# Kernel tuning notes

Measured on AMD Instinct MI355X. Metric: run time of the kernel, lower is better.

Reference implementation:

```python
import jax, jax.numpy as jnp
import numpy as np

N, U, V = 512, 2048, 43          # batch, phoneme seq len, vocab (Phoneme43)
H, K, NCLASS = 512, 10, 512      # hidden, GMM components, 2**bit
EPS = 1e-5


def gru_cell(x, h, wih, whh, bih, bhh):
    # PyTorch GRU gate order: r, z, n
    gi = x @ wih.T + bih          # [N, 3H]
    gh = h @ whh.T + bhh          # [N, 3H]
    gi_r, gi_z, gi_n = jnp.split(gi, 3, axis=1)
    gh_r, gh_z, gh_n = jnp.split(gh, 3, axis=1)
    r = jax.nn.sigmoid(gi_r + gh_r)
    z = jax.nn.sigmoid(gi_z + gh_z)
    n = jnp.tanh(gi_n + r * gh_n)
    return (1.0 - z) * n + z * h


def setup_inputs() -> dict:
    key = jax.random.key(0)
    ks = jax.random.split(key, 20)
    s = 0.05  # keep exp() arguments tame
    inp = {
        "xt": jax.random.normal(ks[0], (N,), jnp.float32),
        "cx": jax.random.uniform(ks[1], (N, U, V), jnp.float32),
        "encoder_hidden": jax.random.normal(ks[2], (1, N, H), jnp.float32),
        "wt_1": jax.random.normal(ks[3], (N, V), jnp.float32) * s,
        "h2t_1": jax.random.normal(ks[4], (1, N, H), jnp.float32),
        "h3t_1": jax.random.uniform(ks[5], (1, N, H), jnp.float32),
        "kappa_t_1": jax.random.uniform(ks[6], (N, K), jnp.float32),
        # learned params
        "Wh1p_w": jax.random.normal(ks[7], (3 * K, H + V), jnp.float32) * s,
        "Wh1p_b": jax.random.normal(ks[8], (3 * K,), jnp.float32) * s,
        "rnn2_wih": jax.random.normal(ks[9], (3 * H, 1 + V), jnp.float32) * s,
        "rnn2_whh": jax.random.normal(ks[10], (3 * H, H), jnp.float32) * s,
        "rnn2_bih": jax.random.normal(ks[11], (3 * H,), jnp.float32) * s,
        "rnn2_bhh": jax.random.normal(ks[12], (3 * H,), jnp.float32) * s,
        "rnn3_wih": jax.random.normal(ks[13], (3 * H, H), jnp.float32) * s,
        "rnn3_whh": jax.random.normal(ks[14], (3 * H, H), jnp.float32) * s,
        "rnn3_bih": jax.random.normal(ks[15], (3 * H,), jnp.float32) * s,
        "rnn3_bhh": jax.random.normal(ks[16], (3 * H,), jnp.float32) * s,
        "Y_w": jax.random.normal(ks[17], (NCLASS, H), jnp.float32) * s,
        "Y_b": jax.random.normal(ks[18], (NCLASS,), jnp.float32) * s,
    }
    return inp


def reference(xt, cx, encoder_hidden, wt_1, h2t_1, h3t_1, kappa_t_1,
              Wh1p_w, Wh1p_b, rnn2_wih, rnn2_whh, rnn2_bih, rnn2_bhh,
              rnn3_wih, rnn3_whh, rnn3_bih, rnn3_bhh, Y_w, Y_b):
    eh = encoder_hidden[0]                                   # [N, H]
    abk = jnp.concatenate([eh, wt_1], axis=1) @ Wh1p_w.T + Wh1p_b  # [N, 3K]
    alpha = jnp.exp(abk[:, :K]) + EPS                        # [N, K]
    beta = jnp.exp(abk[:, K:2 * K]) + EPS                    # [N, K]
    kappa = kappa_t_1 + jnp.exp(abk[:, 2 * K:3 * K])         # [N, K]
    u = jnp.arange(cx.shape[1], dtype=cx.dtype)              # [U]
    # Graves GMM attention window: phi[n,u] = sum_k alpha * exp(-beta*(kappa-u)^2)
    phi = jnp.sum(alpha[:, :, None] *
                  jnp.exp(-beta[:, :, None] * (kappa[:, :, None] - u) ** 2),
                  axis=1)                                    # [N, U]
    wt = jnp.einsum("nuv,nu->nv", cx, phi)                  # [N, V]
    x2 = jnp.concatenate([xt[:, None], wt], axis=1)          # [N, 1+V]
    h2 = gru_cell(x2, h2t_1[0], rnn2_wih, rnn2_whh, rnn2_bih, rnn2_bhh)
    res = h2
    h3 = gru_cell(jax.nn.relu(h2), h3t_1[0], rnn3_wih, rnn3_whh, rnn3_bih, rnn3_bhh)
    out = h3 + res                                           # [N, H]
    dist = jax.nn.relu(out) @ Y_w.T + Y_b                    # [N, n_class]
    dist = dist[:, None, :]                                  # [N, 1, n_class] (transpose(0,1) of [1,N,C])
    return dist, h2[None], h3[None], phi, wt, kappa
```

## Files before the change

kernel.cpp:

```cpp
#include <hip/hip_runtime.h>
#include <math.h>

typedef unsigned short ushortT;
typedef __attribute__((ext_vector_type(8))) short bf16x8;
typedef __attribute__((ext_vector_type(8))) unsigned short u16x8;
typedef __attribute__((ext_vector_type(4))) float f32x4;
typedef float f32x4u __attribute__((ext_vector_type(4), aligned(4)));

#define NN   512
#define UU   2048
#define VV   43
#define HH   512
#define KMIX 10
#define NCLS 512
#define EPSF 1e-5f
#define KCAT 555
#define PLANE 262144

#define OFF_DIST  0
#define OFF_H2    262144
#define OFF_H3    524288
#define OFF_PHI   786432
#define OFF_WT    1835008
#define OFF_KAPPA 1857024

__device__ __forceinline__ ushortT f2bf(float f) {
    unsigned int u = __builtin_bit_cast(unsigned int, f);
    u = (u + 0x7fffu + ((u >> 16) & 1u)) >> 16;
    return (ushortT)u;
}

__device__ __forceinline__ u16x8 cv8(float4 lo, float4 hi) {
    u16x8 o;
    o[0]=f2bf(lo.x); o[1]=f2bf(lo.y); o[2]=f2bf(lo.z); o[3]=f2bf(lo.w);
    o[4]=f2bf(hi.x); o[5]=f2bf(hi.y); o[6]=f2bf(hi.z); o[7]=f2bf(hi.w);
    return o;
}

struct AttnS {
    float x[KCAT];
    float sm[32];
    float aL[KMIX], bL[KMIX], kL[KMIX], um[KMIX];
    float red[4*VV];
    float wtv[VV+1];
};

#define MFMA16(a,b,c) __builtin_amdgcn_mfma_f32_16x16x32_bf16(a,b,c,0,0,0)

template<int NG, int NSA, int NSB, int EPI, int WIK, int MODE>
__device__ __forceinline__ void gemm_body(
    int bj0, int bm0, ushortT* lds0, ushortT* lds1,
    const ushortT* __restrict__ Ai, const float* __restrict__ Wi,
    const float* __restrict__ Ah, const float* __restrict__ Wh,
    const float* __restrict__ bih, const float* __restrict__ bhh,
    const float* __restrict__ hprev, const float* __restrict__ resv,
    float* __restrict__ outF, ushortT* __restrict__ outB,
    const float* __restrict__ Yb, float* __restrict__ preC)
{
    constexpr int NS = NSA + NSB;
    int tid = threadIdx.x, lane = tid & 63, wid = tid >> 6;
    int wm = wid >> 1, wj = wid & 1;
    int fcol = lane & 15, g2 = lane >> 4;
    int arow = tid >> 3, aslot = tid & 7;

    float4 stgA[NG+1][2], stgB[NG+1][2];
    const float4 fz = {0.f, 0.f, 0.f, 0.f};

    auto loadregs = [&](int s, float4 (&dst)[NG+1][2]) {
        if (s < NSA) {
            dst[0][0] = *(const float4*)(Ai + (size_t)(bm0 + arow)*(NSA*64) + s*64 + aslot*8);
#pragma unroll
            for (int q = 1; q <= NG; ++q) {
                int unit = (q-1)*256 + tid;
                int brow = unit >> 3, bslot = unit & 7;
                int gate = brow >> 5, r = brow & 31;
                int col = s*64 + bslot*8;
                const float* src = Wi + (size_t)(gate*512 + bj0 + r)*WIK + col;
                if constexpr (WIK % 64 != 0) {
                    dst[q][0] = (col + 4 <= WIK) ? *(const float4*)src : fz;
                    dst[q][1] = (col + 8 <= WIK) ? *(const float4*)(src + 4) : fz;
                } else {
                    dst[q][0] = *(const float4*)src;
                    dst[q][1] = *(const float4*)(src + 4);
                }
            }
        } else {
            int kb = (s - NSA)*64;
            const float* srcA = Ah + (size_t)(bm0 + arow)*512 + kb + aslot*8;
            dst[0][0] = *(const float4*)srcA;
            dst[0][1] = *(const float4*)(srcA + 4);
#pragma unroll
            for (int q = 1; q <= NG; ++q) {
                int unit = (q-1)*256 + tid;
                int brow = unit >> 3, bslot = unit & 7;
                int gate = brow >> 5, r = brow & 31;
                const float* src = Wh + (size_t)(gate*512 + bj0 + r)*512 + kb + bslot*8;
                dst[q][0] = *(const float4*)src;
                dst[q][1] = *(const float4*)(src + 4);
            }
        }
    };
    auto stow = [&](int s, const float4 (&src)[NG+1][2], ushortT* buf) {
        if (s < NSA) {
            *(float4*)(buf + arow*64 + (aslot ^ (arow & 7))*8) = src[0][0];
        } else {
            *(u16x8*)(buf + arow*64 + (aslot ^ (arow & 7))*8) = cv8(src[0][0], src[0][1]);
        }
#pragma unroll
        for (int q = 1; q <= NG; ++q) {
            int unit = (q-1)*256 + tid;
            int brow = unit >> 3, bslot = unit & 7;
            *(u16x8*)(buf + 2048 + brow*64 + (bslot ^ (brow & 7))*8) = cv8(src[q][0], src[q][1]);
        }
    };

    f32x4 aR = {0.f,0.f,0.f,0.f}, aZ = {0.f,0.f,0.f,0.f};
    f32x4 aN1 = {0.f,0.f,0.f,0.f}, aN2 = {0.f,0.f,0.f,0.f};

    int ra = wm*16 + fcol, rb = wj*16 + fcol;

    loadregs(0, stgA);
    stow(0, stgA, lds0);
    if (NS > 1) loadregs(1, stgB);
    __syncthreads();

#pragma unroll
    for (int s = 0; s < NS; ++s) {
        ushortT* cur = (s & 1) ? lds1 : lds0;
        ushortT* nxt = (s & 1) ? lds0 : lds1;
        if (s + 2 < NS) {
            if (s & 1) loadregs(s + 2, stgB); else loadregs(s + 2, stgA);
        }
        bf16x8 af0 = *(const bf16x8*)(cur + ra*64 + ((g2    ) ^ (ra & 7))*8);
        bf16x8 af1 = *(const bf16x8*)(cur + ra*64 + ((4 + g2) ^ (ra & 7))*8);
        bf16x8 b0[NG], b1[NG];
#pragma unroll
        for (int g = 0; g < NG; ++g) {
            int rbt = g*32 + rb;
            b0[g] = *(const bf16x8*)(cur + 2048 + rbt*64 + ((g2    ) ^ (rbt & 7))*8);
            b1[g] = *(const bf16x8*)(cur + 2048 + rbt*64 + ((4 + g2) ^ (rbt & 7))*8);
        }
        if (s + 1 < NS) {
            if (s & 1) stow(s + 1, stgA, nxt); else stow(s + 1, stgB, nxt);
        }
        aR = MFMA16(af0, b0[0], aR);
        aR = MFMA16(af1, b1[0], aR);
        if constexpr (NG >= 2) {
            aZ = MFMA16(af0, b0[1], aZ);
            aZ = MFMA16(af1, b1[1], aZ);
        }
        if constexpr (NG >= 3) {
            if (s < NSA) {
                aN1 = MFMA16(af0, b0[2], aN1);
                aN1 = MFMA16(af1, b1[2], aN1);
            } else {
                aN2 = MFMA16(af0, b0[2], aN2);
                aN2 = MFMA16(af1, b1[2], aN2);
            }
        }
        __syncthreads();
    }

    int row0 = bm0 + wm*16 + (lane >> 4)*4;
    int col  = bj0 + wj*16 + fcol;

    if constexpr (MODE == 1) {
#pragma unroll
        for (int e = 0; e < 4; ++e) {
            size_t off = (size_t)(row0 + e)*512 + col;
            preC[off]           = aR[e];
            preC[PLANE + off]   = aZ[e];
            preC[2*PLANE + off] = aN2[e];
        }
    } else if constexpr (EPI == 0) {
        float b = Yb[col];
#pragma unroll
        for (int e = 0; e < 4; ++e)
            outF[(size_t)(row0 + e)*512 + col] = aR[e] + b;
    } else {
        float b_r  = bih[col] + bhh[col];
        float b_z  = bih[512 + col] + bhh[512 + col];
        float b_ni = bih[1024 + col];
        float b_nh = bhh[1024 + col];
#pragma unroll
        for (int e = 0; e < 4; ++e) {
            size_t off = (size_t)(row0 + e)*512 + col;
            float gr = aR[e], gz = aZ[e], gnh = aN2[e];
            if constexpr (MODE == 2) {
                gr  += preC[off];
                gz  += preC[PLANE + off];
                gnh  = preC[2*PLANE + off];
            }
            float r  = 1.f/(1.f + __expf(-(gr + b_r)));
            float z  = 1.f/(1.f + __expf(-(gz + b_z)));
            float nn = tanhf(aN1[e] + b_ni + r*(gnh + b_nh));
            float h  = (1.f - z)*nn + z*hprev[off];
            outF[off] = h;
            float xo = (EPI == 2) ? (h + resv[off]) : h;
            outB[off] = f2bf(fmaxf(xo, 0.f));
        }
    }
}

__global__ __launch_bounds__(256) void attn_gh(
    const float* __restrict__ xt, const float* __restrict__ cx,
    const float* __restrict__ eh, const float* __restrict__ wt_1,
    const float* __restrict__ Ww, const float* __restrict__ Wb,
    const float* __restrict__ kappa_prev,
    float* __restrict__ phi_out, float* __restrict__ wt_out,
    float* __restrict__ kappa_out, ushortT* __restrict__ A2,
    const float* __restrict__ h2p, const float* __restrict__ w2hh,
    const float* __restrict__ h3p, const float* __restrict__ w3hh,
    float* __restrict__ gh2C, float* __restrict__ gh3C)
{
    __shared__ __align__(16) ushortT smem[2][4*32*64];
    int bb = blockIdx.x, t = threadIdx.x;

    if (bb >= NN) {
        int gb = bb - NN;
        int sub = gb & 255;
        int bj0 = (sub & 15)*32, bm0 = (sub >> 4)*32;
        if (gb < 256)
            gemm_body<3, 0, 8, 1, 512, 1>(bj0, bm0, &smem[0][0], &smem[1][0],
                nullptr, nullptr, h2p, w2hh, nullptr, nullptr, nullptr, nullptr,
                nullptr, nullptr, nullptr, gh2C);
        else
            gemm_body<3, 0, 8, 1, 512, 1>(bj0, bm0, &smem[0][0], &smem[1][0],
                nullptr, nullptr, h3p, w3hh, nullptr, nullptr, nullptr, nullptr,
                nullptr, nullptr, nullptr, gh3C);
        return;
    }

    AttnS* S = (AttnS*)&smem[0][0];
    int n = bb;
    int lane = t & 63, wid = t >> 6;
    const float* cxn = cx + (size_t)n*UU*VV;

    const float* rowp0 = cxn + (size_t)t*VV;
    f32x4u r0[10]; f32x4u rt0;
#pragma unroll
    for (int q = 0; q < 10; ++q) r0[q] = *(const f32x4u*)(rowp0 + q*4);
    rt0 = *(const f32x4u*)(rowp0 + 39);

    for (int i = t; i < KCAT; i += 256)
        S->x[i] = (i < HH) ? eh[(size_t)n*HH + i] : wt_1[n*VV + (i - HH)];
    __syncthreads();
#pragma unroll
    for (int rr = 0; rr < 8; ++rr) {
        int g = rr*4 + wid;
        float v = 0.f;
        if (g < 30) {
            const float* w = Ww + (size_t)g*KCAT;
#pragma unroll
            for (int q = 0; q < 9; ++q) {
                int i = q*64 + lane;
                if (i < KCAT) v += S->x[i]*w[i];
            }
        }
        v += __shfl_xor(v, 32, 64); v += __shfl_xor(v, 16, 64); v += __shfl_xor(v, 8, 64);
        v += __shfl_xor(v, 4, 64);  v += __shfl_xor(v, 2, 64);  v += __shfl_xor(v, 1, 64);
        if (lane == 0 && g < 30) S->sm[g] = v;
    }
    __syncthreads();
    if (t < 30) {
        float ev = __expf(S->sm[t] + Wb[t]);
        if (t < 10)       S->aL[t] = ev + EPSF;
        else if (t < 20)  S->bL[t-10] = ev + EPSF;
        else { float kap = kappa_prev[n*KMIX + (t-20)] + ev; S->kL[t-20] = kap;
               kappa_out[n*KMIX + (t-20)] = kap; }
    }
    __syncthreads();
    if (t < KMIX)
        S->um[t] = S->kL[t] + sqrtf(fmaxf(60.f + __logf(S->aL[t]), 0.f) / S->bL[t]);
    __syncthreads();
    float ulim = S->um[0];
#pragma unroll
    for (int k = 1; k < KMIX; ++k) ulim = fmaxf(ulim, S->um[k]);
    int nchunks = min(8, (int)(ulim) / 256 + 1);
    nchunks = __builtin_amdgcn_readfirstlane(nchunks);

    float aL[KMIX], bL[KMIX], kL[KMIX];
#pragma unroll
    for (int k = 0; k < KMIX; ++k) { aL[k] = S->aL[k]; bL[k] = S->bL[k]; kL[k] = S->kL[k]; }

    float phi_reg[8];
#pragma unroll
    for (int c = 0; c < 8; ++c) {
        float s = 0.f;
        if ((float)(c*256 + wid*64) <= ulim) {
            int u = c*256 + t; float uu = (float)u;
#pragma unroll
            for (int k = 0; k < KMIX; ++k) { float d = kL[k] - uu; s += aL[k]*__expf(-bL[k]*d*d); }
        }
        phi_reg[c] = s;
        phi_out[(size_t)n*UU + c*256 + t] = s;
    }

    float acc[VV];
    {
        float p = phi_reg[0];
#pragma unroll
        for (int q = 0; q < 10; ++q) {
            acc[q*4+0] = r0[q].x*p; acc[q*4+1] = r0[q].y*p;
            acc[q*4+2] = r0[q].z*p; acc[q*4+3] = r0[q].w*p;
        }
        acc[40] = rt0.y*p; acc[41] = rt0.z*p; acc[42] = rt0.w*p;
    }
#pragma unroll
    for (int c = 1; c < 8; ++c) {
        if (c < nchunks) {
            const float* rowp = cxn + (size_t)(c*256 + t)*VV;
            f32x4u r[10];
#pragma unroll
            for (int q = 0; q < 10; ++q) r[q] = *(const f32x4u*)(rowp + q*4);
            f32x4u rt = *(const f32x4u*)(rowp + 39);
            float p = phi_reg[c];
#pragma unroll
            for (int q = 0; q < 10; ++q) {
                acc[q*4+0] += r[q].x*p; acc[q*4+1] += r[q].y*p;
                acc[q*4+2] += r[q].z*p; acc[q*4+3] += r[q].w*p;
            }
            acc[40] += rt.y*p; acc[41] += rt.z*p; acc[42] += rt.w*p;
        }
    }

#pragma unroll
    for (int v = 0; v < VV; ++v) {
        float val = acc[v];
#pragma unroll
        for (int off = 32; off > 0; off >>= 1) val += __shfl_down(val, off, 64);
        if (lane == 0) S->red[wid*VV + v] = val;
    }
    __syncthreads();
    if (t < VV) {
        float w4 = S->red[t] + S->red[VV+t] + S->red[2*VV+t] + S->red[3*VV+t];
        wt_out[n*VV + t] = w4; S->wtv[t] = w4;
    }
    __syncthreads();
    if (t < 64) {
        float v = (t == 0) ? xt[n] : (t < 44 ? S->wtv[t-1] : 0.f);
        A2[(size_t)n*64 + t] = f2bf(v);
    }
}

template<int NG, int NSA, int NSB, int EPI, int WIK, int MODE>
__global__ __launch_bounds__(256) void gemm_k(
    const ushortT* __restrict__ Ai, const float* __restrict__ Wi,
    const float* __restrict__ Ah, const float* __restrict__ Wh,
    const float* __restrict__ bih, const float* __restrict__ bhh,
    const float* __restrict__ hprev, const float* __restrict__ resv,
    float* __restrict__ outF, ushortT* __restrict__ outB,
    const float* __restrict__ Yb, float* __restrict__ preC)
{
    __shared__ __align__(16) ushortT lds0[(NG+1)*32*64];
    __shared__ __align__(16) ushortT lds1[(NG+1)*32*64];
    gemm_body<NG, NSA, NSB, EPI, WIK, MODE>(
        blockIdx.x*32, blockIdx.y*32, lds0, lds1,
        Ai, Wi, Ah, Wh, bih, bhh, hprev, resv, outF, outB, Yb, preC);
}

extern "C" void kernel_launch(void* const* d_in, const int* in_sizes, int n_in,
                              void* d_out, int out_size, void* d_ws, size_t ws_size,
                              hipStream_t stream)
{
    const float* xt   = (const float*)d_in[0];
    const float* cx   = (const float*)d_in[1];
    const float* eh   = (const float*)d_in[2];
    const float* wt_1 = (const float*)d_in[3];
    const float* h2p  = (const float*)d_in[4];
    const float* h3p  = (const float*)d_in[5];
    const float* kp   = (const float*)d_in[6];
    const float* Ww   = (const float*)d_in[7];
    const float* Wb   = (const float*)d_in[8];
    const float* w2ih = (const float*)d_in[9];
    const float* w2hh = (const float*)d_in[10];
    const float* b2ih = (const float*)d_in[11];
    const float* b2hh = (const float*)d_in[12];
    const float* w3ih = (const float*)d_in[13];
    const float* w3hh = (const float*)d_in[14];
    const float* b3ih = (const float*)d_in[15];
    const float* b3hh = (const float*)d_in[16];
    const float* Yw   = (const float*)d_in[17];
    const float* Yb   = (const float*)d_in[18];

    float* out = (float*)d_out;
    float* dist = out + OFF_DIST;
    float* h2o  = out + OFF_H2;
    float* h3o  = out + OFF_H3;
    float* phi  = out + OFF_PHI;
    float* wto  = out + OFF_WT;
    float* kapo = out + OFF_KAPPA;

    char* p = (char*)d_ws;
    ushortT* A2   = (ushortT*)p;  p += (size_t)512*64*2;
    ushortT* A3i  = (ushortT*)p;  p += (size_t)512*512*2;
    ushortT* Ad   = (ushortT*)p;  p += (size_t)512*512*2;
    float*   gh2C = (float*)p;    p += (size_t)3*PLANE*4;
    float*   gh3C = (float*)p;    p += (size_t)3*PLANE*4;

    attn_gh<<<1024, 256, 0, stream>>>(
        xt, cx, eh, wt_1, Ww, Wb, kp, phi, wto, kapo, A2,
        h2p, w2hh, h3p, w3hh, gh2C, gh3C);
    gemm_k<3, 1, 0, 1, 44, 2><<<dim3(16, 16), 256, 0, stream>>>(
        A2, w2ih, nullptr, nullptr, b2ih, b2hh, h2p, nullptr, h2o, A3i, nullptr, gh2C);
    gemm_k<3, 8, 0, 2, 512, 2><<<dim3(16, 16), 256, 0, stream>>>(
        A3i, w3ih, nullptr, nullptr, b3ih, b3hh, h3p, h2o, h3o, Ad, nullptr, gh3C);
    gemm_k<1, 8, 0, 0, 512, 0><<<dim3(16, 16), 256, 0, stream>>>(
        Ad, Yw, nullptr, nullptr, nullptr, nullptr, nullptr, nullptr, dist, nullptr, Yb, nullptr);
}
```

Before: 49.97 us.

## Fuse three tail GEMM launches into one kernel with per-row-block flag sync

Replaces the three back-to-back GEMM launches (GRU2 input, GRU3 input, output projection) with a single 768-block kernel. Blocks in later stages spin on per-row-block atomic counters until all 16 column blocks of the earlier stage for the same rows are done. The attention kernel resets the flags. This removes two launch gaps and lets later stages start as soon as their rows are ready, but relies on earlier blocks being scheduled first to avoid deadlock, and adds spin-wait overhead.

```diff
diff --git a/kernel.cpp b/kernel.cpp
--- a/kernel.cpp
+++ b/kernel.cpp
@@ -211,10 +211,13 @@
     float* __restrict__ kappa_out, ushortT* __restrict__ A2,
     const float* __restrict__ h2p, const float* __restrict__ w2hh,
     const float* __restrict__ h3p, const float* __restrict__ w3hh,
-    float* __restrict__ gh2C, float* __restrict__ gh3C)
+    float* __restrict__ gh2C, float* __restrict__ gh3C,
+    unsigned* __restrict__ flags)
 {
     __shared__ __align__(16) ushortT smem[2][4*32*64];
     int bb = blockIdx.x, t = threadIdx.x;
+
+    if (bb == 0 && t < 32) flags[t] = 0u;
 
     if (bb >= NN) {
         int gb = bb - NN;
@@ -343,20 +346,61 @@
     }
 }
 
-template<int NG, int NSA, int NSB, int EPI, int WIK, int MODE>
-__global__ __launch_bounds__(256) void gemm_k(
-    const ushortT* __restrict__ Ai, const float* __restrict__ Wi,
-    const float* __restrict__ Ah, const float* __restrict__ Wh,
-    const float* __restrict__ bih, const float* __restrict__ bhh,
-    const float* __restrict__ hprev, const float* __restrict__ resv,
-    float* __restrict__ outF, ushortT* __restrict__ outB,
-    const float* __restrict__ Yb, float* __restrict__ preC)
+__global__ __launch_bounds__(256) void tail_kernel(
+    const ushortT* __restrict__ A2, const float* __restrict__ w2ih,
+    const float* __restrict__ gh2C, const float* __restrict__ b2ih,
+    const float* __restrict__ b2hh, const float* __restrict__ h2p,
+    const float* __restrict__ w3ih, const float* __restrict__ gh3C,
+    const float* __restrict__ b3ih, const float* __restrict__ b3hh,
+    const float* __restrict__ h3p, const float* __restrict__ Yw,
+    const float* __restrict__ Yb,
+    float* __restrict__ h2o, float* __restrict__ h3o,
+    ushortT* __restrict__ A3i, ushortT* __restrict__ Ad,
+    float* __restrict__ dist, unsigned* __restrict__ flagA,
+    unsigned* __restrict__ flagB)
 {
-    __shared__ __align__(16) ushortT lds0[(NG+1)*32*64];
-    __shared__ __align__(16) ushortT lds1[(NG+1)*32*64];
-    gemm_body<NG, NSA, NSB, EPI, WIK, MODE>(
-        blockIdx.x*32, blockIdx.y*32, lds0, lds1,
-        Ai, Wi, Ah, Wh, bih, bhh, hprev, resv, outF, outB, Yb, preC);
+    __shared__ __align__(16) ushortT lds0[4*32*64];
+    __shared__ __align__(16) ushortT lds1[4*32*64];
+    int bb = blockIdx.x, tid = threadIdx.x;
+    int sub = bb & 255;
+    int bj0 = (sub & 15)*32, bm0 = (sub >> 4)*32;
+    int bmIdx = sub >> 4;
+
+    if (bb < 256) {
+        gemm_body<3, 1, 0, 1, 44, 2>(bj0, bm0, lds0, lds1,
+            A2, w2ih, nullptr, nullptr, b2ih, b2hh, h2p, nullptr,
+            h2o, A3i, nullptr, const_cast<float*>(gh2C));
+        __syncthreads();
+        if (tid == 0) {
+            __threadfence();
+            __hip_atomic_fetch_add(flagA + bmIdx, 1u, __ATOMIC_RELEASE, __HIP_MEMORY_SCOPE_AGENT);
+        }
+    } else if (bb < 512) {
+        if (tid == 0) {
+            while (__hip_atomic_load(flagA + bmIdx, __ATOMIC_ACQUIRE, __HIP_MEMORY_SCOPE_AGENT) < 16u)
+                __builtin_amdgcn_s_sleep(8);
+            __threadfence();
+        }
+        __syncthreads();
+        gemm_body<3, 8, 0, 2, 512, 2>(bj0, bm0, lds0, lds1,
+            A3i, w3ih, nullptr, nullptr, b3ih, b3hh, h3p, h2o,
+            h3o, Ad, nullptr, const_cast<float*>(gh3C));
+        __syncthreads();
+        if (tid == 0) {
+            __threadfence();
+            __hip_atomic_fetch_add(flagB + bmIdx, 1u, __ATOMIC_RELEASE, __HIP_MEMORY_SCOPE_AGENT);
+        }
+    } else {
+        if (tid == 0) {
+            while (__hip_atomic_load(flagB + bmIdx, __ATOMIC_ACQUIRE, __HIP_MEMORY_SCOPE_AGENT) < 16u)
+                __builtin_amdgcn_s_sleep(8);
+            __threadfence();
+        }
+        __syncthreads();
+        gemm_body<1, 8, 0, 0, 512, 0>(bj0, bm0, lds0, lds1,
+            Ad, Yw, nullptr, nullptr, nullptr, nullptr, nullptr, nullptr,
+            dist, nullptr, Yb, nullptr);
+    }
 }
 
 extern "C" void kernel_launch(void* const* d_in, const int* in_sizes, int n_in,
@@ -397,14 +441,13 @@
     ushortT* Ad   = (ushortT*)p;  p += (size_t)512*512*2;
     float*   gh2C = (float*)p;    p += (size_t)3*PLANE*4;
     float*   gh3C = (float*)p;    p += (size_t)3*PLANE*4;
+    unsigned* flags = (unsigned*)p;  p += 128;
 
     attn_gh<<<1024, 256, 0, stream>>>(
         xt, cx, eh, wt_1, Ww, Wb, kp, phi, wto, kapo, A2,
-        h2p, w2hh, h3p, w3hh, gh2C, gh3C);
-    gemm_k<3, 1, 0, 1, 44, 2><<<dim3(16, 16), 256, 0, stream>>>(
-        A2, w2ih, nullptr, nullptr, b2ih, b2hh, h2p, nullptr, h2o, A3i, nullptr, gh2C);
-    gemm_k<3, 8, 0, 2, 512, 2><<<dim3(16, 16), 256, 0, stream>>>(
-        A3i, w3ih, nullptr, nullptr, b3ih, b3hh, h3p, h2o, h3o, Ad, nullptr, gh3C);
-    gemm_k<1, 8, 0, 0, 512, 0><<<dim3(16, 16), 256, 0, stream>>>(
-        Ad, Yw, nullptr, nullptr, nullptr, nullptr, nullptr, nullptr, dist, nullptr, Yb, nullptr);
-}
+        h2p, w2hh, h3p, w3hh, gh2C, gh3C, flags);
+    tail_kernel<<<768, 256, 0, stream>>>(
+        A2, w2ih, gh2C, b2ih, b2hh, h2p,
+        w3ih, gh3C, b3ih, b3hh, h3p, Yw, Yb,
+        h2o, h3o, A3i, Ad, dist, flags, flags + 16);
+}
```

Result: slower. 168.8 us (+237.8%).

## Stage cx chunks through LDS with coalesced float4 loads for attention reduction

Applied to the files above, without the earlier changes.

The weighted sum over cx rows no longer has each thread load its own strided 43-float row from global memory. The block now copies 128-row half-chunks into LDS with contiguous float4 loads, then half the threads accumulate from LDS. The goal is better global coalescing for the dominant cx read. The cost is extra barriers per half-chunk, half the threads sitting idle during each accumulate, and dropping the early prefetch of the first chunk that used to overlap with the GMM parameter computation. The red and wtv buffers also move out of the aliased struct, since smem is now reused as the staging buffer.

```diff
diff --git a/kernel.cpp b/kernel.cpp
--- a/kernel.cpp
+++ b/kernel.cpp
@@ -5,7 +5,6 @@
 typedef __attribute__((ext_vector_type(8))) short bf16x8;
 typedef __attribute__((ext_vector_type(8))) unsigned short u16x8;
 typedef __attribute__((ext_vector_type(4))) float f32x4;
-typedef float f32x4u __attribute__((ext_vector_type(4), aligned(4)));
 
 #define NN   512
 #define UU   2048
@@ -41,8 +40,6 @@
     float x[KCAT];
     float sm[32];
     float aL[KMIX], bL[KMIX], kL[KMIX], um[KMIX];
-    float red[4*VV];
-    float wtv[VV+1];
 };
 
 #define MFMA16(a,b,c) __builtin_amdgcn_mfma_f32_16x16x32_bf16(a,b,c,0,0,0)
@@ -214,6 +211,8 @@
     float* __restrict__ gh2C, float* __restrict__ gh3C)
 {
     __shared__ __align__(16) ushortT smem[2][4*32*64];
+    __shared__ float red[4*VV];
+    __shared__ float wtv[VV+1];
     int bb = blockIdx.x, t = threadIdx.x;
 
     if (bb >= NN) {
@@ -236,12 +235,6 @@
     int lane = t & 63, wid = t >> 6;
     const float* cxn = cx + (size_t)n*UU*VV;
 
-    const float* rowp0 = cxn + (size_t)t*VV;
-    f32x4u r0[10]; f32x4u rt0;
-#pragma unroll
-    for (int q = 0; q < 10; ++q) r0[q] = *(const f32x4u*)(rowp0 + q*4);
-    rt0 = *(const f32x4u*)(rowp0 + 39);
-
     for (int i = t; i < KCAT; i += 256)
         S->x[i] = (i < HH) ? eh[(size_t)n*HH + i] : wt_1[n*VV + (i - HH)];
     __syncthreads();
@@ -297,48 +290,47 @@
     }
 
     float acc[VV];
-    {
-        float p = phi_reg[0];
-#pragma unroll
-        for (int q = 0; q < 10; ++q) {
-            acc[q*4+0] = r0[q].x*p; acc[q*4+1] = r0[q].y*p;
-            acc[q*4+2] = r0[q].z*p; acc[q*4+3] = r0[q].w*p;
-        }
-        acc[40] = rt0.y*p; acc[41] = rt0.z*p; acc[42] = rt0.w*p;
-    }
-#pragma unroll
-    for (int c = 1; c < 8; ++c) {
-        if (c < nchunks) {
-            const float* rowp = cxn + (size_t)(c*256 + t)*VV;
-            f32x4u r[10];
-#pragma unroll
-            for (int q = 0; q < 10; ++q) r[q] = *(const f32x4u*)(rowp + q*4);
-            f32x4u rt = *(const f32x4u*)(rowp + 39);
-            float p = phi_reg[c];
-#pragma unroll
-            for (int q = 0; q < 10; ++q) {
-                acc[q*4+0] += r[q].x*p; acc[q*4+1] += r[q].y*p;
-                acc[q*4+2] += r[q].z*p; acc[q*4+3] += r[q].w*p;
-            }
-            acc[40] += rt.y*p; acc[41] += rt.z*p; acc[42] += rt.w*p;
-        }
-    }
+#pragma unroll
+    for (int v = 0; v < VV; ++v) acc[v] = 0.f;
+    float* ch = (float*)&smem[0][0];
+    float4* ch4 = (float4*)ch;
+    int th = t >> 7, tl = t & 127;
+    for (int c = 0; c < nchunks; ++c) {
+#pragma unroll
+        for (int h = 0; h < 2; ++h) {
+            __syncthreads();
+            const float4* src = (const float4*)(cxn + (size_t)(c*256 + h*128)*VV);
+#pragma unroll
+            for (int q = 0; q < 6; ++q) {
+                int i = q*256 + t;
+                if (i < 1376) ch4[i] = src[i];
+            }
+            __syncthreads();
+            if (th == h) {
+                const float* row = ch + tl*VV;
+                float p = phi_reg[c];
+#pragma unroll
+                for (int v = 0; v < VV; ++v) acc[v] += row[v]*p;
+            }
+        }
+    }
+    __syncthreads();
 
 #pragma unroll
     for (int v = 0; v < VV; ++v) {
         float val = acc[v];
 #pragma unroll
         for (int off = 32; off > 0; off >>= 1) val += __shfl_down(val, off, 64);
-        if (lane == 0) S->red[wid*VV + v] = val;
+        if (lane == 0) red[wid*VV + v] = val;
     }
     __syncthreads();
     if (t < VV) {
-        float w4 = S->red[t] + S->red[VV+t] + S->red[2*VV+t] + S->red[3*VV+t];
-        wt_out[n*VV + t] = w4; S->wtv[t] = w4;
+        float w4 = red[t] + red[VV+t] + red[2*VV+t] + red[3*VV+t];
+        wt_out[n*VV + t] = w4; wtv[t] = w4;
     }
     __syncthreads();
     if (t < 64) {
-        float v = (t == 0) ? xt[n] : (t < 44 ? S->wtv[t-1] : 0.f);
+        float v = (t == 0) ? xt[n] : (t < 44 ? wtv[t-1] : 0.f);
         A2[(size_t)n*64 + t] = f2bf(v);
     }
 }
```

Measured after the change: 50.12 us. Within noise of the previous version (+0.3%).
